# Kernel optimization log

Measured on AMD Instinct MI355X. Metric: run time of the kernel, lower is better.

The kernel has to match this reference:

```python
import jax, jax.numpy as jnp
import numpy as np

N_NODES = 50000
N_EDGES = 1600000
IN_CH = 128
HID_CH = 32
HEADS1 = 4
OUT_CH = 64
NEG_SLOPE = 0.2


def setup_inputs() -> dict:
    key = jax.random.key(0)
    ks = jax.random.split(key, 12)
    x = jax.random.normal(ks[0], (N_NODES, IN_CH), dtype=jnp.float32)
    edge_index = jax.random.randint(ks[1], (2, N_EDGES), 0, N_NODES, dtype=jnp.int64)

    def glorot(k, shape):
        fan = shape[0] + shape[-1]
        lim = jnp.sqrt(6.0 / fan).astype(jnp.float32)
        return jax.random.uniform(k, shape, jnp.float32, -lim, lim)

    # conv1: GATConv(IN_CH, HID_CH, heads=4), concat -> HID_CH*4
    W1 = glorot(ks[2], (IN_CH, HEADS1 * HID_CH))
    a_src1 = glorot(ks[3], (HEADS1, HID_CH))
    a_dst1 = glorot(ks[4], (HEADS1, HID_CH))
    b1 = jnp.zeros((HEADS1 * HID_CH,), jnp.float32)
    # conv2: GATConv(HID_CH*4, OUT_CH, heads=1)
    W2 = glorot(ks[5], (HEADS1 * HID_CH, OUT_CH))
    a_src2 = glorot(ks[6], (1, OUT_CH))
    a_dst2 = glorot(ks[7], (1, OUT_CH))
    b2 = jnp.zeros((OUT_CH,), jnp.float32)
    return {"x": x, "edge_index": edge_index, "W1": W1, "a_src1": a_src1,
            "a_dst1": a_dst1, "b1": b1, "W2": W2, "a_src2": a_src2,
            "a_dst2": a_dst2, "b2": b2}


def gat_conv(x, src, dst, W, a_src, a_dst, b, heads, ch, concat, num_nodes):
    # linear transform per head: [N, heads, ch]
    h = (x @ W).reshape(num_nodes, heads, ch)
    # per-node attention logits: [N, heads]
    al_src = jnp.sum(h * a_src[None], axis=-1)
    al_dst = jnp.sum(h * a_dst[None], axis=-1)
    # edge-wise score e_ij = leaky_relu(al_src[j] + al_dst[i]): [E, heads]
    e = jax.nn.leaky_relu(al_src[src] + al_dst[dst], NEG_SLOPE)
    # segment softmax over incoming edges of each dst node (numerically stable)
    m = jax.ops.segment_max(e, dst, num_segments=num_nodes)
    e = jnp.exp(e - m[dst])
    s = jax.ops.segment_sum(e, dst, num_segments=num_nodes)
    alpha = e / (s[dst] + 1e-16)
    # gather source features, weight, scatter-add to dst
    msg = h[src] * alpha[:, :, None]                      # [E, heads, ch]
    out = jax.ops.segment_sum(msg, dst, num_segments=num_nodes)  # [N, heads, ch]
    out = out.reshape(num_nodes, heads * ch) if concat else out.mean(axis=1)
    return out + b


def reference(x, edge_index, W1, a_src1, a_dst1, b1, W2, a_src2, a_dst2, b2):
    n = x.shape[0]
    # add self-loops (PyG GATConv default add_self_loops=True)
    loops = jnp.arange(n, dtype=edge_index.dtype)
    src = jnp.concatenate([edge_index[0], loops])
    dst = jnp.concatenate([edge_index[1], loops])
    h = gat_conv(x, src, dst, W1, a_src1, a_dst1, b1, HEADS1, HID_CH, True, n)
    h = jax.nn.elu(h)
    out = gat_conv(h, src, dst, W2, a_src2, a_dst2, b2, 1, OUT_CH, True, n)
    return out
```

## Files before the change

kernel.cpp:

```cpp
#include <hip/hip_runtime.h>

#define NN 50000
#define NE 1600000
#define ET (NE + NN)
#define NEG 0.2f
#define NBUCK 196
#define CAP 10240
#define NBLK_A ((ET + 4095) / 4096)
#define G1_BLOCKS ((NN + 31) / 32)
#define G1_SPLIT 782

typedef unsigned int uint;

__device__ __forceinline__ float bflo(uint u){ return __uint_as_float(u << 16); }
__device__ __forceinline__ float bfhi(uint u){ return __uint_as_float(u & 0xffff0000u); }
__device__ __forceinline__ uint f2bf2(float lo, float hi){
    uint a = __float_as_uint(lo); a += 0x7fffu + ((a >> 16) & 1u);
    uint b = __float_as_uint(hi); b += 0x7fffu + ((b >> 16) & 1u);
    return (a >> 16) | (b & 0xffff0000u);
}
__device__ __forceinline__ int clampn(int v){ return v < 0 ? 0 : (v >= NN ? NN - 1 : v); }

__device__ __forceinline__ int load_src(const int* ei, int i64, int t){
    return clampn(i64 ? ei[2 * t] : ei[t]);
}
__device__ __forceinline__ int load_dst(const int* ei, int i64, int t){
    return clampn(i64 ? ei[2 * NE + 2 * t] : ei[NE + t]);
}

__global__ void setup_kernel(const int* __restrict__ ei, int* __restrict__ flag, int* __restrict__ gcur){
    __shared__ int sd[256];
    int t = threadIdx.x;
    if (t < NBUCK) gcur[t] = 0;
    sd[t] = ei[2 * (t * 6250) + 1];
    __syncthreads();
    for (int o = 128; o > 0; o >>= 1){
        if (t < o) sd[t] |= sd[t + o];
        __syncthreads();
    }
    if (t == 0) *flag = (sd[0] == 0) ? 1 : 0;
}

__device__ __forceinline__ void bucketA_body(char* smem, int b, const int* __restrict__ ei,
                                             const int* __restrict__ flag, int* __restrict__ gcur,
                                             uint* __restrict__ bdata){
    int* hist = (int*)smem;
    int* base = hist + NBUCK;
    int t = threadIdx.x;
    for (int j = t; j < NBUCK; j += 256) hist[j] = 0;
    __syncthreads();
    int e0 = b * 4096;
    int i64 = *flag;
    int sarr[16], darr[16];
    if (e0 + 4096 <= NE){
        int eb = e0 + t * 16;
        if (i64){
            const int4* s4 = (const int4*)ei + (eb >> 1);
            const int4* d4 = (const int4*)(ei + 2 * NE) + (eb >> 1);
            #pragma unroll
            for (int q = 0; q < 8; ++q){
                int4 v = s4[q]; sarr[2*q] = v.x; sarr[2*q+1] = v.z;
                int4 w = d4[q]; darr[2*q] = w.x; darr[2*q+1] = w.z;
            }
        } else {
            const int4* s4 = (const int4*)ei + (eb >> 2);
            const int4* d4 = (const int4*)(ei + NE) + (eb >> 2);
            #pragma unroll
            for (int q = 0; q < 4; ++q){
                int4 v = s4[q]; sarr[4*q]=v.x; sarr[4*q+1]=v.y; sarr[4*q+2]=v.z; sarr[4*q+3]=v.w;
                int4 w = d4[q]; darr[4*q]=w.x; darr[4*q+1]=w.y; darr[4*q+2]=w.z; darr[4*q+3]=w.w;
            }
        }
        #pragma unroll
        for (int j = 0; j < 16; ++j){ sarr[j] = clampn(sarr[j]); darr[j] = clampn(darr[j]); }
    } else {
        #pragma unroll
        for (int j = 0; j < 16; ++j){
            int e = e0 + t * 16 + j;
            if (e < NE){ sarr[j] = load_src(ei, i64, e); darr[j] = load_dst(ei, i64, e); }
            else if (e < ET){ sarr[j] = e - NE; darr[j] = e - NE; }
            else { sarr[j] = -1; darr[j] = -1; }
        }
    }
    uint vals[16]; int bks[16];
    #pragma unroll
    for (int j = 0; j < 16; ++j){
        if (darr[j] >= 0){
            int bk = darr[j] >> 8;
            bks[j] = bk;
            vals[j] = ((uint)(darr[j] & 255) << 17) | (uint)sarr[j];
            atomicAdd(&hist[bk], 1);
        } else bks[j] = -1;
    }
    __syncthreads();
    for (int j = t; j < NBUCK; j += 256){
        int c = hist[j];
        base[j] = c ? atomicAdd(&gcur[j], c) : 0;
        hist[j] = 0;
    }
    __syncthreads();
    #pragma unroll
    for (int j = 0; j < 16; ++j){
        int bk = bks[j];
        if (bk >= 0){
            int lp = base[bk] + atomicAdd(&hist[bk], 1);
            if (lp < CAP) bdata[(size_t)bk * CAP + lp] = vals[j];
        }
    }
}

__device__ __forceinline__ void bucketB_body(char* smem, int b, const uint* __restrict__ bdata,
                                             const int* __restrict__ gcur, int* __restrict__ offsets,
                                             int* __restrict__ ends, int* __restrict__ csr){
    int* hist = (int*)smem;
    int* excl = hist + 256;
    int* sgb  = excl + 256;
    int t = threadIdx.x;
    int cv = (t < NBUCK) ? gcur[t] : 0; if (cv > CAP) cv = CAP;
    excl[t] = cv;
    __syncthreads();
    for (int o = 1; o < 256; o <<= 1){
        int x = (t >= o) ? excl[t - o] : 0;
        __syncthreads();
        excl[t] += x;
        __syncthreads();
    }
    if (t == b) *sgb = excl[t] - cv;
    __syncthreads();
    int gb = *sgb;
    int n = gcur[b]; if (n > CAP) n = CAP;
    hist[t] = 0;
    __syncthreads();
    const uint* bd = bdata + (size_t)b * CAP;
    for (int i = t; i < n; i += 256)
        atomicAdd(&hist[bd[i] >> 17], 1);
    __syncthreads();
    int v = hist[t];
    excl[t] = v;
    __syncthreads();
    for (int o = 1; o < 256; o <<= 1){
        int x = (t >= o) ? excl[t - o] : 0;
        __syncthreads();
        excl[t] += x;
        __syncthreads();
    }
    int ex = excl[t] - v;
    int node = b * 256 + t;
    if (node < NN){ offsets[node] = gb + ex; ends[node] = gb + ex + v; }
    __syncthreads();
    hist[t] = ex;
    __syncthreads();
    for (int i = t; i < n; i += 256){
        uint val = bd[i];
        int lp = atomicAdd(&hist[val >> 17], 1);
        csr[gb + lp] = (int)(val & 0x1FFFFu);
    }
}

__device__ __forceinline__ void gemm1_body(char* smem, int gb, const float* __restrict__ x,
                                           const float* __restrict__ W1, const float* __restrict__ as1,
                                           const float* __restrict__ ad1, uint* __restrict__ h1b,
                                           float* __restrict__ als, float* __restrict__ ald){
    float* xs = (float*)smem;
    int t = threadIdx.x;
    int row0 = gb * 32;
    const float4* x4 = (const float4*)x;
    float4* xs4 = (float4*)xs;
    #pragma unroll
    for (int j = 0; j < 4; ++j){
        int idx = t + j * 256;
        int gi = row0 * 32 + idx;
        if (gi < NN * 32) xs4[idx] = x4[gi];
    }
    __syncthreads();
    int rg = t >> 5, cg = t & 31;
    float acc[4][4];
    #pragma unroll
    for (int i = 0; i < 4; ++i)
        #pragma unroll
        for (int c = 0; c < 4; ++c) acc[i][c] = 0.f;
    const float4* W4 = (const float4*)W1;
    for (int k4 = 0; k4 < 32; ++k4){
        int k = k4 * 4;
        float4 xv[4];
        #pragma unroll
        for (int i = 0; i < 4; ++i) xv[i] = xs4[(rg * 4 + i) * 32 + k4];
        float4 w0 = W4[(k + 0) * 32 + cg];
        float4 w1 = W4[(k + 1) * 32 + cg];
        float4 w2 = W4[(k + 2) * 32 + cg];
        float4 w3 = W4[(k + 3) * 32 + cg];
        #pragma unroll
        for (int i = 0; i < 4; ++i){
            acc[i][0] = fmaf(xv[i].x, w0.x, acc[i][0]);
            acc[i][1] = fmaf(xv[i].x, w0.y, acc[i][1]);
            acc[i][2] = fmaf(xv[i].x, w0.z, acc[i][2]);
            acc[i][3] = fmaf(xv[i].x, w0.w, acc[i][3]);
            acc[i][0] = fmaf(xv[i].y, w1.x, acc[i][0]);
            acc[i][1] = fmaf(xv[i].y, w1.y, acc[i][1]);
            acc[i][2] = fmaf(xv[i].y, w1.z, acc[i][2]);
            acc[i][3] = fmaf(xv[i].y, w1.w, acc[i][3]);
            acc[i][0] = fmaf(xv[i].z, w2.x, acc[i][0]);
            acc[i][1] = fmaf(xv[i].z, w2.y, acc[i][1]);
            acc[i][2] = fmaf(xv[i].z, w2.z, acc[i][2]);
            acc[i][3] = fmaf(xv[i].z, w2.w, acc[i][3]);
            acc[i][0] = fmaf(xv[i].w, w3.x, acc[i][0]);
            acc[i][1] = fmaf(xv[i].w, w3.y, acc[i][1]);
            acc[i][2] = fmaf(xv[i].w, w3.z, acc[i][2]);
            acc[i][3] = fmaf(xv[i].w, w3.w, acc[i][3]);
        }
    }
    int h = cg >> 3, c0 = (cg & 7) * 4;
    const float* ash = as1 + h * 32 + c0;
    const float* adh = ad1 + h * 32 + c0;
    float as0 = ash[0], as1v = ash[1], as2v = ash[2], as3v = ash[3];
    float ad0 = adh[0], ad1v = adh[1], ad2v = adh[2], ad3v = adh[3];
    #pragma unroll
    for (int i = 0; i < 4; ++i){
        int n = row0 + rg * 4 + i;
        if (n < NN){
            ((uint2*)h1b)[n * 32 + cg] = make_uint2(f2bf2(acc[i][0], acc[i][1]),
                                                    f2bf2(acc[i][2], acc[i][3]));
            float ps = acc[i][0] * as0 + acc[i][1] * as1v + acc[i][2] * as2v + acc[i][3] * as3v;
            float pd = acc[i][0] * ad0 + acc[i][1] * ad1v + acc[i][2] * ad2v + acc[i][3] * ad3v;
            ps += __shfl_xor(ps, 1); pd += __shfl_xor(pd, 1);
            ps += __shfl_xor(ps, 2); pd += __shfl_xor(pd, 2);
            ps += __shfl_xor(ps, 4); pd += __shfl_xor(pd, 4);
            if ((cg & 7) == 0){ als[n * 4 + h] = ps; ald[n * 4 + h] = pd; }
        }
    }
}

__global__ __launch_bounds__(256) void k1_kernel(const int* __restrict__ ei, const int* __restrict__ flag,
                                                 int* __restrict__ gcur, uint* __restrict__ bdata,
                                                 const float* __restrict__ x, const float* __restrict__ W1,
                                                 const float* __restrict__ as1, const float* __restrict__ ad1,
                                                 uint* __restrict__ h1b, float* __restrict__ als,
                                                 float* __restrict__ ald){
    __shared__ __align__(16) char smem[32 * 128 * 4];
    if ((int)blockIdx.x < NBLK_A) bucketA_body(smem, blockIdx.x, ei, flag, gcur, bdata);
    else gemm1_body(smem, blockIdx.x - NBLK_A, x, W1, as1, ad1, h1b, als, ald);
}

__global__ __launch_bounds__(256) void k2_kernel(const uint* __restrict__ bdata, const int* __restrict__ gcur,
                                                 int* __restrict__ offsets, int* __restrict__ ends,
                                                 int* __restrict__ csr,
                                                 const float* __restrict__ x, const float* __restrict__ W1,
                                                 const float* __restrict__ as1, const float* __restrict__ ad1,
                                                 uint* __restrict__ h1b, float* __restrict__ als,
                                                 float* __restrict__ ald){
    __shared__ __align__(16) char smem[32 * 128 * 4];
    if ((int)blockIdx.x < NBUCK) bucketB_body(smem, blockIdx.x, bdata, gcur, offsets, ends, csr);
    else gemm1_body(smem, blockIdx.x - NBUCK + G1_SPLIT, x, W1, as1, ad1, h1b, als, ald);
}

__global__ __launch_bounds__(256) void edge1_kernel(const int* __restrict__ offs, const int* __restrict__ ends,
                                                    const int* __restrict__ csr, const uint* __restrict__ h1b,
                                                    const float* __restrict__ als, const float* __restrict__ ald,
                                                    const float* __restrict__ b1, uint* __restrict__ helub){
    __shared__ int   ss[4][64];
    __shared__ float sw[4][64][4];
    int t = threadIdx.x, wave = t >> 6, lane = t & 63;
    int node = blockIdx.x * 4 + wave;
    int begin = offs[node], end = ends[node];
    int deg = end - begin;
    int eg = lane >> 4, cl = lane & 15, hh = cl >> 2;
    float4 ad = ((const float4*)ald)[node];
    const float4* als4 = (const float4*)als;
    const uint4* h1b4 = (const uint4*)h1b;

    float ws0 = 0, ws1 = 0, ws2 = 0, ws3 = 0;
    float acc[8];
    #pragma unroll
    for (int i = 0; i < 8; ++i) acc[i] = 0.f;
    bool fast = (deg <= 64);

    if (fast){
        float w0 = 0, w1 = 0, w2 = 0, w3 = 0;
        int s0 = 0;
        if (lane < deg){
            s0 = csr[begin + lane];
            float4 a = als4[s0];
            float e0 = a.x + ad.x; e0 = e0 > 0.f ? e0 : NEG * e0; w0 = __expf(e0);
            float e1 = a.y + ad.y; e1 = e1 > 0.f ? e1 : NEG * e1; w1 = __expf(e1);
            float e2 = a.z + ad.z; e2 = e2 > 0.f ? e2 : NEG * e2; w2 = __expf(e2);
            float e3 = a.w + ad.w; e3 = e3 > 0.f ? e3 : NEG * e3; w3 = __expf(e3);
            ws0 = w0; ws1 = w1; ws2 = w2; ws3 = w3;
        }
        ss[wave][lane] = s0;
        sw[wave][lane][0] = w0; sw[wave][lane][1] = w1;
        sw[wave][lane][2] = w2; sw[wave][lane][3] = w3;
        __threadfence_block();
        int dlim = (deg + 3) & ~3;
        int j = 0;
        for (; j + 16 <= dlim; j += 16){
            int sj[4]; float wj[4]; uint4 v[4];
            #pragma unroll
            for (int q = 0; q < 4; ++q){
                sj[q] = ss[wave][j + 4 * q + eg];
                wj[q] = sw[wave][j + 4 * q + eg][hh];
            }
            #pragma unroll
            for (int q = 0; q < 4; ++q) v[q] = h1b4[(size_t)sj[q] * 16 + cl];
            #pragma unroll
            for (int q = 0; q < 4; ++q){
                acc[0] = fmaf(wj[q], bflo(v[q].x), acc[0]);
                acc[1] = fmaf(wj[q], bfhi(v[q].x), acc[1]);
                acc[2] = fmaf(wj[q], bflo(v[q].y), acc[2]);
                acc[3] = fmaf(wj[q], bfhi(v[q].y), acc[3]);
                acc[4] = fmaf(wj[q], bflo(v[q].z), acc[4]);
                acc[5] = fmaf(wj[q], bfhi(v[q].z), acc[5]);
                acc[6] = fmaf(wj[q], bflo(v[q].w), acc[6]);
                acc[7] = fmaf(wj[q], bfhi(v[q].w), acc[7]);
            }
        }
        for (; j < dlim; j += 4){
            int sj = ss[wave][j + eg]; float wj = sw[wave][j + eg][hh];
            uint4 v = h1b4[(size_t)sj * 16 + cl];
            acc[0] = fmaf(wj, bflo(v.x), acc[0]);
            acc[1] = fmaf(wj, bfhi(v.x), acc[1]);
            acc[2] = fmaf(wj, bflo(v.y), acc[2]);
            acc[3] = fmaf(wj, bfhi(v.y), acc[3]);
            acc[4] = fmaf(wj, bflo(v.z), acc[4]);
            acc[5] = fmaf(wj, bfhi(v.z), acc[5]);
            acc[6] = fmaf(wj, bflo(v.w), acc[6]);
            acc[7] = fmaf(wj, bfhi(v.w), acc[7]);
        }
    } else {
        for (int base = begin; base < end; base += 64){
            int n = end - base; if (n > 64) n = 64;
            float w0 = 0, w1 = 0, w2 = 0, w3 = 0; int sv = 0;
            if (lane < n){
                sv = csr[base + lane];
                float4 a = als4[sv];
                float f0 = a.x + ad.x; f0 = f0 > 0.f ? f0 : NEG * f0; w0 = __expf(f0);
                float f1 = a.y + ad.y; f1 = f1 > 0.f ? f1 : NEG * f1; w1 = __expf(f1);
                float f2 = a.z + ad.z; f2 = f2 > 0.f ? f2 : NEG * f2; w2 = __expf(f2);
                float f3 = a.w + ad.w; f3 = f3 > 0.f ? f3 : NEG * f3; w3 = __expf(f3);
                ws0 += w0; ws1 += w1; ws2 += w2; ws3 += w3;
            }
            __threadfence_block();
            ss[wave][lane] = sv;
            sw[wave][lane][0] = w0; sw[wave][lane][1] = w1;
            sw[wave][lane][2] = w2; sw[wave][lane][3] = w3;
            __threadfence_block();
            int dlim = (n + 3) & ~3;
            for (int j = 0; j < dlim; j += 4){
                int sj = ss[wave][j + eg]; float wj = sw[wave][j + eg][hh];
                uint4 v = h1b4[(size_t)sj * 16 + cl];
                acc[0] = fmaf(wj, bflo(v.x), acc[0]);
                acc[1] = fmaf(wj, bfhi(v.x), acc[1]);
                acc[2] = fmaf(wj, bflo(v.y), acc[2]);
                acc[3] = fmaf(wj, bfhi(v.y), acc[3]);
                acc[4] = fmaf(wj, bflo(v.z), acc[4]);
                acc[5] = fmaf(wj, bfhi(v.z), acc[5]);
                acc[6] = fmaf(wj, bflo(v.w), acc[6]);
                acc[7] = fmaf(wj, bfhi(v.w), acc[7]);
            }
        }
    }
    for (int o = 32; o > 0; o >>= 1){
        ws0 += __shfl_xor(ws0, o); ws1 += __shfl_xor(ws1, o);
        ws2 += __shfl_xor(ws2, o); ws3 += __shfl_xor(ws3, o);
    }
    #pragma unroll
    for (int i = 0; i < 8; ++i){
        acc[i] += __shfl_xor(acc[i], 16);
        acc[i] += __shfl_xor(acc[i], 32);
    }
    if (eg == 0){
        float wsum = hh == 0 ? ws0 : (hh == 1 ? ws1 : (hh == 2 ? ws2 : ws3));
        float inv = 1.f / (wsum + 1e-16f);
        int c0 = cl * 8;
        float o[8];
        #pragma unroll
        for (int i = 0; i < 8; ++i){
            float v = acc[i] * inv + b1[c0 + i];
            o[i] = v > 0.f ? v : __expf(v) - 1.f;
        }
        uint4 pk = make_uint4(f2bf2(o[0], o[1]), f2bf2(o[2], o[3]),
                              f2bf2(o[4], o[5]), f2bf2(o[6], o[7]));
        ((uint4*)helub)[(size_t)node * 16 + cl] = pk;
    }
}

__global__ __launch_bounds__(256) void gemm2_kernel(const uint* __restrict__ helub, const float* __restrict__ W2,
                                                    const float* __restrict__ as2, const float* __restrict__ ad2,
                                                    uint* __restrict__ h2b, float* __restrict__ als2,
                                                    float* __restrict__ ald2){
    __shared__ float W2s[128 * 64];
    __shared__ uint  hsu[64 * 65];
    int t = threadIdx.x;
    const float4* W24 = (const float4*)W2;
    float4* W2s4 = (float4*)W2s;
    #pragma unroll
    for (int j = 0; j < 8; ++j){ int idx = t + j * 256; W2s4[idx] = W24[idx]; }
    int row0 = blockIdx.x * 64;
    const uint4* hb4 = (const uint4*)helub;
    #pragma unroll
    for (int j = 0; j < 4; ++j){
        int idx = t + j * 256;
        int gi = row0 * 16 + idx;
        if (gi < NN * 16){
            uint4 v = hb4[gi];
            int r = idx >> 4, kq = idx & 15;
            uint* dst = hsu + r * 65 + kq * 4;
            dst[0] = v.x; dst[1] = v.y; dst[2] = v.z; dst[3] = v.w;
        }
    }
    __syncthreads();
    int rg = t >> 4, cg = t & 15;
    float acc[4][4];
    #pragma unroll
    for (int i = 0; i < 4; ++i)
        #pragma unroll
        for (int c = 0; c < 4; ++c) acc[i][c] = 0.f;
    const float4* W2sR = (const float4*)W2s;
    for (int k2 = 0; k2 < 64; ++k2){
        uint hv[4];
        #pragma unroll
        for (int i = 0; i < 4; ++i) hv[i] = hsu[(rg * 4 + i) * 65 + k2];
        float4 wa = W2sR[(2 * k2) * 16 + cg];
        float4 wb = W2sR[(2 * k2 + 1) * 16 + cg];
        #pragma unroll
        for (int i = 0; i < 4; ++i){
            float xl = bflo(hv[i]), xh = bfhi(hv[i]);
            acc[i][0] = fmaf(xl, wa.x, acc[i][0]);
            acc[i][1] = fmaf(xl, wa.y, acc[i][1]);
            acc[i][2] = fmaf(xl, wa.z, acc[i][2]);
            acc[i][3] = fmaf(xl, wa.w, acc[i][3]);
            acc[i][0] = fmaf(xh, wb.x, acc[i][0]);
            acc[i][1] = fmaf(xh, wb.y, acc[i][1]);
            acc[i][2] = fmaf(xh, wb.z, acc[i][2]);
            acc[i][3] = fmaf(xh, wb.w, acc[i][3]);
        }
    }
    int c0 = cg * 4;
    float s0 = as2[c0], s1 = as2[c0 + 1], s2 = as2[c0 + 2], s3 = as2[c0 + 3];
    float d0 = ad2[c0], d1 = ad2[c0 + 1], d2 = ad2[c0 + 2], d3 = ad2[c0 + 3];
    #pragma unroll
    for (int i = 0; i < 4; ++i){
        int n = row0 + rg * 4 + i;
        if (n < NN){
            ((uint2*)h2b)[n * 16 + cg] = make_uint2(f2bf2(acc[i][0], acc[i][1]),
                                                    f2bf2(acc[i][2], acc[i][3]));
            float ps = acc[i][0] * s0 + acc[i][1] * s1 + acc[i][2] * s2 + acc[i][3] * s3;
            float pd = acc[i][0] * d0 + acc[i][1] * d1 + acc[i][2] * d2 + acc[i][3] * d3;
            ps += __shfl_xor(ps, 1); pd += __shfl_xor(pd, 1);
            ps += __shfl_xor(ps, 2); pd += __shfl_xor(pd, 2);
            ps += __shfl_xor(ps, 4); pd += __shfl_xor(pd, 4);
            ps += __shfl_xor(ps, 8); pd += __shfl_xor(pd, 8);
            if (cg == 0){ als2[n] = ps; ald2[n] = pd; }
        }
    }
}

__global__ __launch_bounds__(256) void edge2_kernel(const int* __restrict__ offs, const int* __restrict__ ends,
                                                    const int* __restrict__ csr, const uint* __restrict__ h2b,
                                                    const float* __restrict__ als, const float* __restrict__ ald,
                                                    const float* __restrict__ b2, float* __restrict__ out){
    __shared__ int   ss2[4][64];
    __shared__ float sw2[4][64];
    int t = threadIdx.x, wave = t >> 6, lane = t & 63;
    int node = blockIdx.x * 4 + wave;
    int begin = offs[node], end = ends[node];
    int deg = end - begin;
    int eg = lane >> 3, cl = lane & 7;
    float adv = ald[node];
    const uint4* h2p4 = (const uint4*)h2b;
    float wsl = 0.f;
    float acc[8] = {0.f, 0.f, 0.f, 0.f, 0.f, 0.f, 0.f, 0.f};
    bool fast = (deg <= 64);
    if (fast){
        float w = 0.f; int sv = 0;
        if (lane < deg){
            sv = csr[begin + lane];
            float e = als[sv] + adv; e = e > 0.f ? e : NEG * e;
            w = __expf(e); wsl = w;
        }
        ss2[wave][lane] = sv;
        sw2[wave][lane] = w;
        __threadfence_block();
        int dlim = (deg + 7) & ~7;
        int j = 0;
        for (; j + 16 <= dlim; j += 16){
            int sj0 = ss2[wave][j + eg],     sj1 = ss2[wave][j + 8 + eg];
            float wj0 = sw2[wave][j + eg],   wj1 = sw2[wave][j + 8 + eg];
            uint4 v0 = h2p4[(size_t)sj0 * 8 + cl];
            uint4 v1 = h2p4[(size_t)sj1 * 8 + cl];
            acc[0] = fmaf(wj0, bflo(v0.x), acc[0]); acc[1] = fmaf(wj0, bfhi(v0.x), acc[1]);
            acc[2] = fmaf(wj0, bflo(v0.y), acc[2]); acc[3] = fmaf(wj0, bfhi(v0.y), acc[3]);
            acc[4] = fmaf(wj0, bflo(v0.z), acc[4]); acc[5] = fmaf(wj0, bfhi(v0.z), acc[5]);
            acc[6] = fmaf(wj0, bflo(v0.w), acc[6]); acc[7] = fmaf(wj0, bfhi(v0.w), acc[7]);
            acc[0] = fmaf(wj1, bflo(v1.x), acc[0]); acc[1] = fmaf(wj1, bfhi(v1.x), acc[1]);
            acc[2] = fmaf(wj1, bflo(v1.y), acc[2]); acc[3] = fmaf(wj1, bfhi(v1.y), acc[3]);
            acc[4] = fmaf(wj1, bflo(v1.z), acc[4]); acc[5] = fmaf(wj1, bfhi(v1.z), acc[5]);
            acc[6] = fmaf(wj1, bflo(v1.w), acc[6]); acc[7] = fmaf(wj1, bfhi(v1.w), acc[7]);
        }
        for (; j < dlim; j += 8){
            int sj = ss2[wave][j + eg]; float wj = sw2[wave][j + eg];
            uint4 v = h2p4[(size_t)sj * 8 + cl];
            acc[0] = fmaf(wj, bflo(v.x), acc[0]); acc[1] = fmaf(wj, bfhi(v.x), acc[1]);
            acc[2] = fmaf(wj, bflo(v.y), acc[2]); acc[3] = fmaf(wj, bfhi(v.y), acc[3]);
            acc[4] = fmaf(wj, bflo(v.z), acc[4]); acc[5] = fmaf(wj, bfhi(v.z), acc[5]);
            acc[6] = fmaf(wj, bflo(v.w), acc[6]); acc[7] = fmaf(wj, bfhi(v.w), acc[7]);
        }
    } else {
        for (int base = begin; base < end; base += 64){
            int n = end - base; if (n > 64) n = 64;
            float w = 0.f; int sv = 0;
            if (lane < n){
                sv = csr[base + lane];
                float e = als[sv] + adv; e = e > 0.f ? e : NEG * e;
                w = __expf(e); wsl += w;
            }
            __threadfence_block();
            ss2[wave][lane] = sv;
            sw2[wave][lane] = w;
            __threadfence_block();
            int dlim = (n + 7) & ~7;
            for (int j = 0; j < dlim; j += 8){
                int sj = ss2[wave][j + eg]; float wj = sw2[wave][j + eg];
                uint4 v = h2p4[(size_t)sj * 8 + cl];
                acc[0] = fmaf(wj, bflo(v.x), acc[0]); acc[1] = fmaf(wj, bfhi(v.x), acc[1]);
                acc[2] = fmaf(wj, bflo(v.y), acc[2]); acc[3] = fmaf(wj, bfhi(v.y), acc[3]);
                acc[4] = fmaf(wj, bflo(v.z), acc[4]); acc[5] = fmaf(wj, bfhi(v.z), acc[5]);
                acc[6] = fmaf(wj, bflo(v.w), acc[6]); acc[7] = fmaf(wj, bfhi(v.w), acc[7]);
            }
        }
    }
    for (int o = 32; o > 0; o >>= 1) wsl += __shfl_xor(wsl, o);
    #pragma unroll
    for (int i = 0; i < 8; ++i){
        acc[i] += __shfl_xor(acc[i], 8);
        acc[i] += __shfl_xor(acc[i], 16);
        acc[i] += __shfl_xor(acc[i], 32);
    }
    if (eg == 0){
        float inv = 1.f / (wsl + 1e-16f);
        int c0 = cl * 8;
        ((float4*)out)[node * 16 + cl * 2]     = make_float4(acc[0] * inv + b2[c0],
                                                             acc[1] * inv + b2[c0 + 1],
                                                             acc[2] * inv + b2[c0 + 2],
                                                             acc[3] * inv + b2[c0 + 3]);
        ((float4*)out)[node * 16 + cl * 2 + 1] = make_float4(acc[4] * inv + b2[c0 + 4],
                                                             acc[5] * inv + b2[c0 + 5],
                                                             acc[6] * inv + b2[c0 + 6],
                                                             acc[7] * inv + b2[c0 + 7]);
    }
}


extern "C" void kernel_launch(void* const* d_in, const int* in_sizes, int n_in,
                              void* d_out, int out_size, void* d_ws, size_t ws_size,
                              hipStream_t stream){
    const float* x   = (const float*)d_in[0];
    const int*   ei  = (const int*)d_in[1];
    const float* W1  = (const float*)d_in[2];
    const float* as1 = (const float*)d_in[3];
    const float* ad1 = (const float*)d_in[4];
    const float* b1  = (const float*)d_in[5];
    const float* W2  = (const float*)d_in[6];
    const float* as2 = (const float*)d_in[7];
    const float* ad2 = (const float*)d_in[8];
    const float* b2  = (const float*)d_in[9];
    float* out = (float*)d_out;

    char* p = (char*)d_ws;
    auto alloc = [&](size_t bytes)->void*{
        void* r = (void*)p;
        p += (bytes + 255) & ~(size_t)255;
        return r;
    };
    int*   flag     = (int*)alloc(4);
    int*   gcur     = (int*)alloc(NBUCK * 4);
    int*   offsets  = (int*)alloc(NN * 4);
    int*   endsv    = (int*)alloc(NN * 4);
    void*  ualias   = alloc((size_t)NN * 64 * 4);
    uint*  bdata    = (uint*)ualias;
    uint*  helub    = (uint*)ualias;
    int*   csr      = (int*)alloc((size_t)ET * 4);
    uint*  h1b      = (uint*)alloc((size_t)NN * 64 * 4);
    float* als1     = (float*)alloc((size_t)NN * 4 * 4);
    float* ald1     = (float*)alloc((size_t)NN * 4 * 4);
    uint*  h2b      = (uint*)alloc((size_t)NN * 32 * 4);
    float* als2     = (float*)alloc((size_t)NN * 4);
    float* ald2     = (float*)alloc((size_t)NN * 4);
    size_t need = (size_t)(p - (char*)d_ws);

    if (ws_size < need){
        hipMemsetAsync(d_out, 0, (size_t)out_size * 4, stream);
        return;
    }

    setup_kernel<<<1, 256, 0, stream>>>(ei, flag, gcur);
    k1_kernel<<<NBLK_A + G1_SPLIT, 256, 0, stream>>>(ei, flag, gcur, bdata,
                                                     x, W1, as1, ad1, h1b, als1, ald1);
    k2_kernel<<<NBUCK + (G1_BLOCKS - G1_SPLIT), 256, 0, stream>>>(bdata, gcur, offsets, endsv, csr,
                                                                  x, W1, as1, ad1, h1b, als1, ald1);
    edge1_kernel<<<NN / 4, 256, 0, stream>>>(offsets, endsv, csr, h1b, als1, ald1, b1, helub);
    gemm2_kernel<<<(NN + 63) / 64, 256, 0, stream>>>(helub, W2, as2, ad2, h2b, als2, ald2);
    edge2_kernel<<<NN / 4, 256, 0, stream>>>(offsets, endsv, csr, h2b, als2, ald2, b2, out);
}
```

Before: 251.9 us.

## Drop setup kernel, fold int64 detection into bucket blocks, vectorize bucket reads

Removes the single-block setup kernel: gcur is now zeroed with hipMemsetAsync and each bucketing block detects the int64 edge-index layout itself with a shared-memory OR reduction. The second bucketing pass reads bucket data as uint4 and issues four atomics per load. gemm2 no longer stages W2 in shared memory and reads it straight from global memory, relying on the cache. This saves a launch and reduces LDS use, at the cost of a redundant per-block reduction and uncached global weight loads in the inner loop.

```diff
diff --git a/kernel.cpp b/kernel.cpp
--- a/kernel.cpp
+++ b/kernel.cpp
@@ -28,29 +28,22 @@
     return clampn(i64 ? ei[2 * NE + 2 * t] : ei[NE + t]);
 }
 
-__global__ void setup_kernel(const int* __restrict__ ei, int* __restrict__ flag, int* __restrict__ gcur){
-    __shared__ int sd[256];
-    int t = threadIdx.x;
-    if (t < NBUCK) gcur[t] = 0;
-    sd[t] = ei[2 * (t * 6250) + 1];
-    __syncthreads();
-    for (int o = 128; o > 0; o >>= 1){
-        if (t < o) sd[t] |= sd[t + o];
-        __syncthreads();
-    }
-    if (t == 0) *flag = (sd[0] == 0) ? 1 : 0;
-}
-
 __device__ __forceinline__ void bucketA_body(char* smem, int b, const int* __restrict__ ei,
-                                             const int* __restrict__ flag, int* __restrict__ gcur,
-                                             uint* __restrict__ bdata){
+                                             int* __restrict__ gcur, uint* __restrict__ bdata){
     int* hist = (int*)smem;
     int* base = hist + NBUCK;
     int t = threadIdx.x;
+    hist[t] = ei[2 * (t * 6250) + 1];
+    __syncthreads();
+    for (int o = 128; o > 0; o >>= 1){
+        if (t < o) hist[t] |= hist[t + o];
+        __syncthreads();
+    }
+    int i64 = (hist[0] == 0) ? 1 : 0;
+    __syncthreads();
     for (int j = t; j < NBUCK; j += 256) hist[j] = 0;
     __syncthreads();
     int e0 = b * 4096;
-    int i64 = *flag;
     int sarr[16], darr[16];
     if (e0 + 4096 <= NE){
         int eb = e0 + t * 16;
@@ -132,7 +125,16 @@
     hist[t] = 0;
     __syncthreads();
     const uint* bd = bdata + (size_t)b * CAP;
-    for (int i = t; i < n; i += 256)
+    const uint4* bd4 = (const uint4*)bd;
+    int n4 = n >> 2;
+    for (int i = t; i < n4; i += 256){
+        uint4 v = bd4[i];
+        atomicAdd(&hist[v.x >> 17], 1);
+        atomicAdd(&hist[v.y >> 17], 1);
+        atomicAdd(&hist[v.z >> 17], 1);
+        atomicAdd(&hist[v.w >> 17], 1);
+    }
+    for (int i = 4 * n4 + t; i < n; i += 256)
         atomicAdd(&hist[bd[i] >> 17], 1);
     __syncthreads();
     int v = hist[t];
@@ -150,7 +152,15 @@
     __syncthreads();
     hist[t] = ex;
     __syncthreads();
-    for (int i = t; i < n; i += 256){
+    for (int i = t; i < n4; i += 256){
+        uint4 w = bd4[i];
+        int lp;
+        lp = atomicAdd(&hist[w.x >> 17], 1); csr[gb + lp] = (int)(w.x & 0x1FFFFu);
+        lp = atomicAdd(&hist[w.y >> 17], 1); csr[gb + lp] = (int)(w.y & 0x1FFFFu);
+        lp = atomicAdd(&hist[w.z >> 17], 1); csr[gb + lp] = (int)(w.z & 0x1FFFFu);
+        lp = atomicAdd(&hist[w.w >> 17], 1); csr[gb + lp] = (int)(w.w & 0x1FFFFu);
+    }
+    for (int i = 4 * n4 + t; i < n; i += 256){
         uint val = bd[i];
         int lp = atomicAdd(&hist[val >> 17], 1);
         csr[gb + lp] = (int)(val & 0x1FFFFu);
@@ -230,14 +240,14 @@
     }
 }
 
-__global__ __launch_bounds__(256) void k1_kernel(const int* __restrict__ ei, const int* __restrict__ flag,
+__global__ __launch_bounds__(256) void k1_kernel(const int* __restrict__ ei,
                                                  int* __restrict__ gcur, uint* __restrict__ bdata,
                                                  const float* __restrict__ x, const float* __restrict__ W1,
                                                  const float* __restrict__ as1, const float* __restrict__ ad1,
                                                  uint* __restrict__ h1b, float* __restrict__ als,
                                                  float* __restrict__ ald){
     __shared__ __align__(16) char smem[32 * 128 * 4];
-    if ((int)blockIdx.x < NBLK_A) bucketA_body(smem, blockIdx.x, ei, flag, gcur, bdata);
+    if ((int)blockIdx.x < NBLK_A) bucketA_body(smem, blockIdx.x, ei, gcur, bdata);
     else gemm1_body(smem, blockIdx.x - NBLK_A, x, W1, as1, ad1, h1b, als, ald);
 }
 
@@ -387,13 +397,8 @@
                                                     const float* __restrict__ as2, const float* __restrict__ ad2,
                                                     uint* __restrict__ h2b, float* __restrict__ als2,
                                                     float* __restrict__ ald2){
-    __shared__ float W2s[128 * 64];
-    __shared__ uint  hsu[64 * 65];
+    __shared__ uint hsu[64 * 65];
     int t = threadIdx.x;
-    const float4* W24 = (const float4*)W2;
-    float4* W2s4 = (float4*)W2s;
-    #pragma unroll
-    for (int j = 0; j < 8; ++j){ int idx = t + j * 256; W2s4[idx] = W24[idx]; }
     int row0 = blockIdx.x * 64;
     const uint4* hb4 = (const uint4*)helub;
     #pragma unroll
@@ -414,13 +419,13 @@
     for (int i = 0; i < 4; ++i)
         #pragma unroll
         for (int c = 0; c < 4; ++c) acc[i][c] = 0.f;
-    const float4* W2sR = (const float4*)W2s;
+    const float4* W24 = (const float4*)W2;
     for (int k2 = 0; k2 < 64; ++k2){
         uint hv[4];
         #pragma unroll
         for (int i = 0; i < 4; ++i) hv[i] = hsu[(rg * 4 + i) * 65 + k2];
-        float4 wa = W2sR[(2 * k2) * 16 + cg];
-        float4 wb = W2sR[(2 * k2 + 1) * 16 + cg];
+        float4 wa = W24[(2 * k2) * 16 + cg];
+        float4 wb = W24[(2 * k2 + 1) * 16 + cg];
         #pragma unroll
         for (int i = 0; i < 4; ++i){
             float xl = bflo(hv[i]), xh = bfhi(hv[i]);
@@ -571,7 +576,6 @@
         p += (bytes + 255) & ~(size_t)255;
         return r;
     };
-    int*   flag     = (int*)alloc(4);
     int*   gcur     = (int*)alloc(NBUCK * 4);
     int*   offsets  = (int*)alloc(NN * 4);
     int*   endsv    = (int*)alloc(NN * 4);
@@ -592,8 +596,8 @@
         return;
     }
 
-    setup_kernel<<<1, 256, 0, stream>>>(ei, flag, gcur);
-    k1_kernel<<<NBLK_A + G1_SPLIT, 256, 0, stream>>>(ei, flag, gcur, bdata,
+    hipMemsetAsync(gcur, 0, NBUCK * 4, stream);
+    k1_kernel<<<NBLK_A + G1_SPLIT, 256, 0, stream>>>(ei, gcur, bdata,
                                                      x, W1, as1, ad1, h1b, als1, ald1);
     k2_kernel<<<NBUCK + (G1_BLOCKS - G1_SPLIT), 256, 0, stream>>>(bdata, gcur, offsets, endsv, csr,
                                                                   x, W1, as1, ad1, h1b, als1, ald1);
```

Result: no change. 255.3 us (+1.3%).
